# Kernel optimization log

Measured on AMD Instinct MI355X. Metric: run time of the kernel, lower is better.

The kernel has to match this reference:

```python
import jax, jax.numpy as jnp
import numpy as np

N, E, F, H, G = 50000, 1600000, 128, 128, 64
EPS = 1e-5  # BatchNorm eps


def setup_inputs() -> dict:
    key = jax.random.key(0)
    ks = jax.random.split(key, 16)
    x = jax.random.normal(ks[0], (N, F), dtype=jnp.float32)
    edge_index = jax.random.randint(ks[1], (2, E), 0, N, dtype=jnp.int64)
    batch = jnp.sort(jax.random.randint(ks[2], (N,), 0, G, dtype=jnp.int64))
    inp = {
        'x': x, 'edge_index': edge_index, 'batch': batch,
        'W1': jax.random.normal(ks[3], (F, H), dtype=jnp.float32) / np.sqrt(F),
        'b1': jnp.zeros((H,), jnp.float32),
        'bn1_gamma': jax.random.uniform(ks[4], (H,), jnp.float32, 0.5, 1.5),
        'bn1_beta': jax.random.normal(ks[5], (H,), jnp.float32) * 0.1,
        'bn1_mean': jax.random.normal(ks[6], (H,), jnp.float32) * 0.1,
        'bn1_var': jax.random.uniform(ks[7], (H,), jnp.float32, 0.5, 1.5),
        'W2': jax.random.normal(ks[8], (H, H), dtype=jnp.float32) / np.sqrt(H),
        'b2': jnp.zeros((H,), jnp.float32),
        'bn2_gamma': jax.random.uniform(ks[9], (H,), jnp.float32, 0.5, 1.5),
        'bn2_beta': jax.random.normal(ks[10], (H,), jnp.float32) * 0.1,
        'bn2_mean': jax.random.normal(ks[11], (H,), jnp.float32) * 0.1,
        'bn2_var': jax.random.uniform(ks[12], (H,), jnp.float32, 0.5, 1.5),
        'att_w': jax.random.normal(ks[13], (H, 1), dtype=jnp.float32) / np.sqrt(H),
        'cls_w': jax.random.normal(ks[14], (1, H), dtype=jnp.float32) / np.sqrt(H),
        'cls_b': jnp.zeros((1,), jnp.float32),
    }
    return inp


def gcn_conv(h, W, b, src, dst, n):
    # PyG GCNConv: linear, add self-loops, symmetric D^{-1/2}(A+I)D^{-1/2} aggregation, bias.
    hw = h @ W                                   # [n, H]
    loops = jnp.arange(n, dtype=src.dtype)
    s = jnp.concatenate([src, loops])
    d = jnp.concatenate([dst, loops])
    deg = jax.ops.segment_sum(jnp.ones_like(d, dtype=hw.dtype), d, num_segments=n)
    dis = jnp.where(deg > 0, jax.lax.rsqrt(deg), 0.0)
    norm = dis[s] * dis[d]                       # [E+n]
    msgs = hw[s] * norm[:, None]                 # gather + scale (memory-bound)
    return jax.ops.segment_sum(msgs, d, num_segments=n) + b


def batch_norm(h, gamma, beta, mean, var):
    return (h - mean) * gamma * jax.lax.rsqrt(var + EPS) + beta


def reference(x, edge_index, batch, W1, b1, bn1_gamma, bn1_beta, bn1_mean, bn1_var,
              W2, b2, bn2_gamma, bn2_beta, bn2_mean, bn2_var, att_w, cls_w, cls_b):
    n = x.shape[0]
    src, dst = edge_index[0], edge_index[1]
    # eval mode: dropout and edge-dropout are no-ops; BN uses running stats
    h = gcn_conv(x, W1, b1, src, dst, n)
    h = jax.nn.relu(batch_norm(h, bn1_gamma, bn1_beta, bn1_mean, bn1_var))
    h = gcn_conv(h, W2, b2, src, dst, n)
    h = jax.nn.relu(batch_norm(h, bn2_gamma, bn2_beta, bn2_mean, bn2_var))
    att = jax.nn.sigmoid(h @ att_w)              # [n, 1]
    g = jax.ops.segment_sum(h * att, batch, num_segments=G)  # [G, H]
    logits = g @ cls_w.T + cls_b                 # [G, 1]
    return logits, att
```

## Files before the change

kernel.cpp:

```cpp
#include <hip/hip_runtime.h>
#include <math.h>

#define NN 50000
#define HID 128
#define NG 64
#define BN_EPS 1e-5f

typedef __attribute__((ext_vector_type(8))) short short8;
typedef __attribute__((ext_vector_type(4))) float f32x4;

__device__ inline unsigned pack_bf2(float a, float b) {
    union { float f; unsigned u; } ua, ub;
    ua.f = a; ub.f = b;
    unsigned x = ua.u, y = ub.u;
    x += 0x7fffu + ((x >> 16) & 1u);
    y += 0x7fffu + ((y >> 16) & 1u);
    return (x >> 16) | (y & 0xffff0000u);
}
__device__ inline unsigned short bf16_1(float x) {
    union { float f; unsigned u; } v;
    v.f = x;
    unsigned r = v.u + 0x7fffu + ((v.u >> 16) & 1u);
    return (unsigned short)(r >> 16);
}
__device__ inline float2 unpack_bf2(unsigned v) {
    union { unsigned u; float f; } a, b;
    a.u = v << 16;
    b.u = v & 0xffff0000u;
    return make_float2(a.f, b.f);
}

#define NBKT 256
#define ETILE 8192
#define CAP   8192
#define ASTR 136

__global__ __launch_bounds__(128) void k_prep0(const float* __restrict__ W1,
                                               const float* __restrict__ W2,
                                               unsigned short* __restrict__ wt1,
                                               unsigned short* __restrict__ wt2,
                                               int* __restrict__ bcurP,
                                               const float* __restrict__ cls_b,
                                               float* __restrict__ logits) {
    int b = blockIdx.x;
    int t = threadIdx.x;
    if (b < 256) {
        int k = b & 127;
        const float* W = (b < 128) ? W1 : W2;
        unsigned short* wt = (b < 128) ? wt1 : wt2;
        wt[t * 128 + k] = bf16_1(W[k * 128 + t]);
    } else {
        #pragma unroll
        for (int i = 0; i < 32; ++i) bcurP[t * 32 + i] = 0;
        if (t < NG) logits[t] = cls_b[0];
    }
}

__global__ __launch_bounds__(256) void k_distribute(const int* __restrict__ src,
                                                    const int* __restrict__ dst,
                                                    int* __restrict__ bcurP,
                                                    unsigned* __restrict__ bpacked,
                                                    int E, int K) {
    __shared__ int h[NBKT];
    int t = threadIdx.x;
    h[t] = 0;
    __syncthreads();
    int base = blockIdx.x * ETILE;
    for (int i = 0; i < ETILE / 256; ++i) {
        int e = base + i * 256 + t;
        if (e < E) atomicAdd(&h[dst[e] / K], 1);
    }
    __syncthreads();
    int c = h[t];
    int my = (c > 0) ? atomicAdd(&bcurP[t * 16], c) : 0;
    __syncthreads();
    h[t] = my;
    __syncthreads();
    for (int i = 0; i < ETILE / 256; ++i) {
        int e = base + i * 256 + t;
        if (e < E) {
            int d = dst[e];
            int bkt = d / K;
            int p = atomicAdd(&h[bkt], 1);
            bpacked[(size_t)bkt * CAP + p] = ((unsigned)d << 16) | (unsigned)src[e];
        }
    }
}

__global__ __launch_bounds__(256) void k_csr_gemm1(const unsigned* __restrict__ bpacked,
                                                   const int* __restrict__ bcurP,
                                                   int* __restrict__ row_ptr,
                                                   int* __restrict__ degA,
                                                   float* __restrict__ dis,
                                                   int* __restrict__ col_idx,
                                                   const float* __restrict__ x,
                                                   const unsigned short* __restrict__ wt1,
                                                   unsigned short* __restrict__ zb,
                                                   int n, int K) {
    __shared__ unsigned short A[64][ASTR];
    __shared__ int cnt[NBKT];
    __shared__ int sA[NBKT];
    __shared__ int cur[NBKT];
    int t = threadIdx.x;
    int b = blockIdx.x;

    if (b >= NBKT) {
        int row0 = (b - NBKT) * 64;
        #pragma unroll
        for (int i = 0; i < 8; ++i) {
            int idx = t + i * 256;
            int r = idx >> 5;
            int c4 = (idx & 31) * 4;
            float4 v = make_float4(0.f, 0.f, 0.f, 0.f);
            if (row0 + r < n) v = *(const float4*)&x[(size_t)(row0 + r) * 128 + c4];
            uint2 p;
            p.x = pack_bf2(v.x, v.y);
            p.y = pack_bf2(v.z, v.w);
            *(uint2*)&A[r][c4] = p;
        }
        __syncthreads();
        int lane = t & 63;
        int wave = t >> 6;
        int m = lane & 15;
        int quad = lane >> 4;
        int r0 = wave * 16;
        short8 a[4];
        #pragma unroll
        for (int kt = 0; kt < 4; ++kt)
            a[kt] = *(const short8*)&A[r0 + m][kt * 32 + quad * 8];
        f32x4 acc[8];
        #pragma unroll
        for (int ct = 0; ct < 8; ++ct) acc[ct] = (f32x4){0.f, 0.f, 0.f, 0.f};
        short8 bcur[4], bnxt[4];
        {
            const unsigned short* wb = &wt1[(size_t)m * 128 + quad * 8];
            #pragma unroll
            for (int kt = 0; kt < 4; ++kt) bcur[kt] = *(const short8*)(wb + kt * 32);
        }
        #pragma unroll
        for (int ct = 0; ct < 8; ++ct) {
            if (ct < 7) {
                const unsigned short* wb = &wt1[(size_t)((ct + 1) * 16 + m) * 128 + quad * 8];
                #pragma unroll
                for (int kt = 0; kt < 4; ++kt) bnxt[kt] = *(const short8*)(wb + kt * 32);
            }
            #pragma unroll
            for (int kt = 0; kt < 4; ++kt)
                acc[ct] = __builtin_amdgcn_mfma_f32_16x16x32_bf16(a[kt], bcur[kt], acc[ct], 0, 0, 0);
            #pragma unroll
            for (int kt = 0; kt < 4; ++kt) bcur[kt] = bnxt[kt];
        }
        __syncthreads();
        #pragma unroll
        for (int ct = 0; ct < 8; ++ct) {
            int col = ct * 16 + m;
            #pragma unroll
            for (int reg = 0; reg < 4; ++reg)
                A[r0 + quad * 4 + reg][col] = bf16_1(acc[ct][reg]);
        }
        __syncthreads();
        #pragma unroll
        for (int i = 0; i < 4; ++i) {
            int idx = t + i * 256;
            int r = idx >> 4;
            int c8 = (idx & 15) * 8;
            int grow = row0 + r;
            if (grow < n)
                *(uint4*)&zb[(size_t)grow * 128 + c8] = *(const uint4*)&A[r][c8];
        }
        return;
    }

    int node0 = b * K;
    int nn = n - node0;
    if (nn > K) nn = K;
    if (nn < 0) nn = 0;
    int e0 = b * CAP;
    int e1 = e0 + bcurP[b * 16];
    cnt[t] = 0;
    __syncthreads();
    for (int e = e0 + t; e < e1; e += 256) {
        int ld = (int)(bpacked[e] >> 16) - node0;
        atomicAdd(&cnt[ld], 1);
    }
    __syncthreads();
    int c = cnt[t];
    sA[t] = c;
    __syncthreads();
    for (int off = 1; off < NBKT; off <<= 1) {
        int v = (t >= off) ? sA[t - off] : 0;
        __syncthreads();
        sA[t] += v;
        __syncthreads();
    }
    int rp = e0 + sA[t] - c;
    cur[t] = rp;
    if (t < nn) {
        row_ptr[node0 + t] = rp;
        degA[node0 + t] = c;
        dis[node0 + t] = rsqrtf((float)(c + 1));
    }
    __syncthreads();
    for (int e = e0 + t; e < e1; e += 256) {
        unsigned v = bpacked[e];
        int ld = (int)(v >> 16) - node0;
        int p = atomicAdd(&cur[ld], 1);
        col_idx[p] = (int)(v & 0xFFFFu);
    }
}


__device__ inline void gather4wide(const unsigned short* __restrict__ hwsb,
                                   const int* __restrict__ col_idx,
                                   int e0, int deg, int md,
                                   int sl, int part, bool active,
                                   float* acc8) {
    int cidx = (active && sl < deg) ? col_idx[e0 + sl] : 0;
    for (int it0 = 0; it0 < md; it0 += 16) {
        int nx = it0 + 16;
        int cidx_next = (active && (nx + sl) < deg && nx < md) ? col_idx[e0 + nx + sl] : 0;
        uint4 vv[16];
        #pragma unroll
        for (int j = 0; j < 16; ++j) {
            int s = __shfl(cidx, (part << 4) + j);
            vv[j] = (it0 + j < deg)
                        ? *(const uint4*)(hwsb + ((size_t)s << 7) + (sl << 3))
                        : make_uint4(0, 0, 0, 0);
        }
        #pragma unroll
        for (int j = 0; j < 16; ++j) {
            const unsigned* w = (const unsigned*)&vv[j];
            #pragma unroll
            for (int i2 = 0; i2 < 4; ++i2) {
                float2 f = unpack_bf2(w[i2]);
                acc8[2 * i2]     += f.x;
                acc8[2 * i2 + 1] += f.y;
            }
        }
        cidx = cidx_next;
    }
}

__device__ inline void gather4wide_scaled(const unsigned short* __restrict__ zb,
                                          const int* __restrict__ col_idx,
                                          const float* __restrict__ dis,
                                          int e0, int deg, int md,
                                          int sl, int part, bool active,
                                          float* acc8) {
    int cidx = (active && sl < deg) ? col_idx[e0 + sl] : 0;
    float cdis = (active && sl < deg) ? dis[cidx] : 0.f;
    for (int it0 = 0; it0 < md; it0 += 16) {
        int nx = it0 + 16;
        bool okn = (active && (nx + sl) < deg && nx < md);
        int cidx_next = okn ? col_idx[e0 + nx + sl] : 0;
        float cdis_next = okn ? dis[cidx_next] : 0.f;
        uint4 vv[16];
        float dsj[16];
        #pragma unroll
        for (int j = 0; j < 16; ++j) {
            int s = __shfl(cidx, (part << 4) + j);
            dsj[j] = __shfl(cdis, (part << 4) + j);
            vv[j] = (it0 + j < deg)
                        ? *(const uint4*)(zb + ((size_t)s << 7) + (sl << 3))
                        : make_uint4(0, 0, 0, 0);
        }
        #pragma unroll
        for (int j = 0; j < 16; ++j) {
            const unsigned* w = (const unsigned*)&vv[j];
            #pragma unroll
            for (int i2 = 0; i2 < 4; ++i2) {
                float2 f = unpack_bf2(w[i2]);
                acc8[2 * i2]     = fmaf(f.x, dsj[j], acc8[2 * i2]);
                acc8[2 * i2 + 1] = fmaf(f.y, dsj[j], acc8[2 * i2 + 1]);
            }
        }
        cidx = cidx_next;
        cdis = cdis_next;
    }
}


__global__ __launch_bounds__(256) void k_agg1_gemm2(const unsigned short* __restrict__ zb,
                                                    const int* __restrict__ row_ptr,
                                                    const int* __restrict__ degA,
                                                    const int* __restrict__ col_idx,
                                                    const float* __restrict__ dis,
                                                    const float* __restrict__ bias,
                                                    const float* __restrict__ gamma,
                                                    const float* __restrict__ beta,
                                                    const float* __restrict__ mean,
                                                    const float* __restrict__ var,
                                                    const unsigned short* __restrict__ wt2,
                                                    unsigned short* __restrict__ hwsb2, int n) {
    __shared__ unsigned short H1[16][ASTR];
    __shared__ unsigned short C2[16][ASTR];
    int t = threadIdx.x;
    int wave = t >> 6, lane = t & 63;
    int sl = lane & 15, part = lane >> 4;
    int d = blockIdx.x * 16 + wave * 4 + part;
    bool active = (d < n);
    int e0 = 0, deg = 0;
    if (active) {
        e0 = row_ptr[d];
        deg = degA[d];
    }
    int md = deg;
    md = max(md, __shfl_xor(md, 16));
    md = max(md, __shfl_xor(md, 32));

    float acc8[8] = {0, 0, 0, 0, 0, 0, 0, 0};
    gather4wide_scaled(zb, col_idx, dis, e0, deg, md, sl, part, active, acc8);

    unsigned outw[4] = {0, 0, 0, 0};
    if (active) {
        float dd = dis[d];
        uint4 v = *(const uint4*)(zb + ((size_t)d << 7) + (sl << 3));
        const unsigned* w = (const unsigned*)&v;
        #pragma unroll
        for (int i2 = 0; i2 < 4; ++i2) {
            float2 f = unpack_bf2(w[i2]);
            acc8[2 * i2]     = fmaf(f.x, dd, acc8[2 * i2]);
            acc8[2 * i2 + 1] = fmaf(f.y, dd, acc8[2 * i2 + 1]);
        }
        int f0 = sl << 3;
        #pragma unroll
        for (int i2 = 0; i2 < 4; ++i2) {
            int f = f0 + 2 * i2;
            float2 bv = *(const float2*)&bias[f];
            float2 gm = *(const float2*)&gamma[f];
            float2 bt = *(const float2*)&beta[f];
            float2 mn = *(const float2*)&mean[f];
            float2 vr = *(const float2*)&var[f];
            float vx = acc8[2 * i2] * dd + bv.x;
            float vy = acc8[2 * i2 + 1] * dd + bv.y;
            float sx = gm.x * rsqrtf(vr.x + BN_EPS);
            float sy = gm.y * rsqrtf(vr.y + BN_EPS);
            float rx = fmaxf((vx - mn.x) * sx + bt.x, 0.f);
            float ry = fmaxf((vy - mn.y) * sy + bt.y, 0.f);
            outw[i2] = pack_bf2(rx, ry);
        }
    }
    int local = wave * 4 + part;
    *(uint4*)&H1[local][sl << 3] = *(uint4*)outw;
    __syncthreads();

    int m = sl;
    int quad = part;
    short8 a2[4];
    #pragma unroll
    for (int kt = 0; kt < 4; ++kt)
        a2[kt] = *(const short8*)&H1[m][kt * 32 + quad * 8];

    f32x4 acc2[2];
    acc2[0] = (f32x4){0.f, 0.f, 0.f, 0.f};
    acc2[1] = (f32x4){0.f, 0.f, 0.f, 0.f};
    #pragma unroll
    for (int i = 0; i < 2; ++i) {
        int ct = wave * 2 + i;
        const unsigned short* wb = &wt2[(size_t)(ct * 16 + m) * 128 + quad * 8];
        #pragma unroll
        for (int kt = 0; kt < 4; ++kt) {
            short8 b = *(const short8*)(wb + kt * 32);
            acc2[i] = __builtin_amdgcn_mfma_f32_16x16x32_bf16(a2[kt], b, acc2[i], 0, 0, 0);
        }
    }
    int gr = blockIdx.x * 16 + quad * 4;
    float ds2[4];
    #pragma unroll
    for (int reg = 0; reg < 4; ++reg)
        ds2[reg] = (gr + reg < n) ? dis[gr + reg] : 0.f;
    #pragma unroll
    for (int i = 0; i < 2; ++i) {
        int col = (wave * 2 + i) * 16 + m;
        #pragma unroll
        for (int reg = 0; reg < 4; ++reg)
            C2[quad * 4 + reg][col] = bf16_1(acc2[i][reg] * ds2[reg]);
    }
    __syncthreads();
    {
        int r = t >> 4;
        int c8 = (t & 15) * 8;
        int grow = blockIdx.x * 16 + r;
        if (grow < n)
            *(uint4*)&hwsb2[(size_t)grow * 128 + c8] = *(const uint4*)&C2[r][c8];
    }
}


__global__ __launch_bounds__(256) void k_agg2_att_logit(const unsigned short* __restrict__ hwsb,
                                                        const int* __restrict__ row_ptr,
                                                        const int* __restrict__ degA,
                                                        const int* __restrict__ col_idx,
                                                        const float* __restrict__ dis,
                                                        const float* __restrict__ bias,
                                                        const float* __restrict__ gamma,
                                                        const float* __restrict__ beta,
                                                        const float* __restrict__ mean,
                                                        const float* __restrict__ var,
                                                        const int* __restrict__ batch,
                                                        const float* __restrict__ att_w,
                                                        const float* __restrict__ cls_w,
                                                        float* __restrict__ att_out,
                                                        float* __restrict__ logits, int n) {
    __shared__ int   sg[16];
    __shared__ float sv[16];
    int t = threadIdx.x;
    int wave = t >> 6, lane = t & 63;
    int sl = lane & 15, part = lane >> 4;
    int d = blockIdx.x * 16 + wave * 4 + part;
    bool active = (d < n);
    int e0 = 0, deg = 0;
    if (active) {
        e0 = row_ptr[d];
        deg = degA[d];
    }
    int md = deg;
    md = max(md, __shfl_xor(md, 16));
    md = max(md, __shfl_xor(md, 32));

    float acc8[8] = {0, 0, 0, 0, 0, 0, 0, 0};
    gather4wide(hwsb, col_idx, e0, deg, md, sl, part, active, acc8);

    int g = -1;
    float contrib = 0.f;
    float p = 0.f, q = 0.f;
    if (active) {
        uint4 v = *(const uint4*)(hwsb + ((size_t)d << 7) + (sl << 3));
        const unsigned* w = (const unsigned*)&v;
        #pragma unroll
        for (int i2 = 0; i2 < 4; ++i2) {
            float2 f = unpack_bf2(w[i2]);
            acc8[2 * i2]     += f.x;
            acc8[2 * i2 + 1] += f.y;
        }
        float dd = dis[d];
        int f0 = sl << 3;
        #pragma unroll
        for (int i2 = 0; i2 < 4; ++i2) {
            int f = f0 + 2 * i2;
            float2 bv = *(const float2*)&bias[f];
            float2 gm = *(const float2*)&gamma[f];
            float2 bt = *(const float2*)&beta[f];
            float2 mn = *(const float2*)&mean[f];
            float2 vr = *(const float2*)&var[f];
            float vx = acc8[2 * i2] * dd + bv.x;
            float vy = acc8[2 * i2 + 1] * dd + bv.y;
            float sx = gm.x * rsqrtf(vr.x + BN_EPS);
            float sy = gm.y * rsqrtf(vr.y + BN_EPS);
            float rx = fmaxf((vx - mn.x) * sx + bt.x, 0.f);
            float ry = fmaxf((vy - mn.y) * sy + bt.y, 0.f);
            float2 aw = *(const float2*)&att_w[f];
            float2 cw = *(const float2*)&cls_w[f];
            p += rx * aw.x + ry * aw.y;
            q += rx * cw.x + ry * cw.y;
        }
    }
    #pragma unroll
    for (int off = 1; off < 16; off <<= 1) {
        p += __shfl_xor(p, off);
        q += __shfl_xor(q, off);
    }
    if (active) {
        float a = 1.f / (1.f + expf(-p));
        if (sl == 0) att_out[d] = a;
        g = batch[d];
        contrib = a * q;
    }
    if (sl == 0) {
        sg[wave * 4 + part] = g;
        sv[wave * 4 + part] = contrib;
    }
    __syncthreads();
    if (t == 0) {
        int cur = -1;
        float acc = 0.f;
        #pragma unroll
        for (int i = 0; i < 16; ++i) {
            int gi = sg[i];
            if (gi < 0) continue;
            if (gi != cur) {
                if (cur >= 0) atomicAdd(&logits[cur], acc);
                cur = gi;
                acc = 0.f;
            }
            acc += sv[i];
        }
        if (cur >= 0) atomicAdd(&logits[cur], acc);
    }
}


extern "C" void kernel_launch(void* const* d_in, const int* in_sizes, int n_in,
                              void* d_out, int out_size, void* d_ws, size_t ws_size,
                              hipStream_t stream) {
    const float* x   = (const float*)d_in[0];
    const int*   ei  = (const int*)d_in[1];
    const int*   bat = (const int*)d_in[2];
    const float* W1  = (const float*)d_in[3];
    const float* b1  = (const float*)d_in[4];
    const float* g1  = (const float*)d_in[5];
    const float* bt1 = (const float*)d_in[6];
    const float* mn1 = (const float*)d_in[7];
    const float* vr1 = (const float*)d_in[8];
    const float* W2  = (const float*)d_in[9];
    const float* b2  = (const float*)d_in[10];
    const float* g2  = (const float*)d_in[11];
    const float* bt2 = (const float*)d_in[12];
    const float* mn2 = (const float*)d_in[13];
    const float* vr2 = (const float*)d_in[14];
    const float* attw = (const float*)d_in[15];
    const float* clsw = (const float*)d_in[16];
    const float* clsb = (const float*)d_in[17];

    int E = in_sizes[1] / 2;
    int n = in_sizes[2];
    const int* src = ei;
    const int* dst = ei + E;
    int K = (n + NBKT - 1) / NBKT;

    char* ws = (char*)d_ws;
    auto alloc = [&](size_t bytes) {
        void* p = (void*)ws;
        ws += (bytes + 255) & ~(size_t)255;
        return p;
    };
    int*            bcurP   = (int*)alloc(NBKT * 16 * 4);
    unsigned*       bpacked = (unsigned*)alloc((size_t)NBKT * CAP * 4);
    int*            row_ptr = (int*)alloc((size_t)n * 4);
    int*            degA    = (int*)alloc((size_t)n * 4);
    int*            col_idx = (int*)alloc((size_t)NBKT * CAP * 4);
    float*          dis     = (float*)alloc((size_t)n * 4);
    unsigned short* zb      = (unsigned short*)alloc((size_t)n * 128 * 2);
    unsigned short* hwsb2   = (unsigned short*)alloc((size_t)n * 128 * 2);
    unsigned short* wt1     = (unsigned short*)alloc(128 * 128 * 2);
    unsigned short* wt2     = (unsigned short*)alloc(128 * 128 * 2);

    float* out = (float*)d_out;
    int etiles = (E + ETILE - 1) / ETILE;
    int gb = (n + 63) / 64;
    int ab = (n + 15) / 16;

    k_prep0<<<257, 128, 0, stream>>>(W1, W2, wt1, wt2, bcurP, clsb, out);
    k_distribute<<<etiles, 256, 0, stream>>>(src, dst, bcurP, bpacked, E, K);
    k_csr_gemm1<<<NBKT + gb, 256, 0, stream>>>(bpacked, bcurP, row_ptr, degA, dis,
                                               col_idx, x, wt1, zb, n, K);
    k_agg1_gemm2<<<ab, 256, 0, stream>>>(zb, row_ptr, degA, col_idx, dis,
                                         b1, g1, bt1, mn1, vr1, wt2, hwsb2, n);
    k_agg2_att_logit<<<ab, 256, 0, stream>>>(hwsb2, row_ptr, degA, col_idx, dis,
                                             b2, g2, bt2, mn2, vr2, bat, attw, clsw,
                                             out + NG, out, n);
}
```

Baseline: 287.6 us.

## Stage bucketed edges in shared memory and flush coalesced chunks in distribute

Replaces the two-pass count-then-scatter edge distribution with a single pass. Each block stages packed edges per bucket in LDS buffers, with a direct global atomic fallback on overflow. Full 16-entry groups are flushed with vectorized contiguous writes. The aim is to avoid the second read of dst and the scattered 4-byte global stores. The cost is more block-wide syncs, more global atomics, and edge order within a bucket that can vary between runs.

```diff
diff --git a/kernel.cpp b/kernel.cpp
--- a/kernel.cpp
+++ b/kernel.cpp
@@ -31,9 +31,11 @@
 }
 
 #define NBKT 256
-#define ETILE 8192
 #define CAP   8192
 #define ASTR 136
+#define DBUF  48
+#define DBATCH 2048
+#define DBLOCKS 192
 
 __global__ __launch_bounds__(128) void k_prep0(const float* __restrict__ W1,
                                                const float* __restrict__ W2,
@@ -58,32 +60,65 @@
 
 __global__ __launch_bounds__(256) void k_distribute(const int* __restrict__ src,
                                                     const int* __restrict__ dst,
-                                                    int* __restrict__ bcurP,
+                                                    int* __restrict__ gcurP,
                                                     unsigned* __restrict__ bpacked,
                                                     int E, int K) {
-    __shared__ int h[NBKT];
+    __shared__ unsigned buf[NBKT][DBUF];
+    __shared__ int cnt[NBKT];
     int t = threadIdx.x;
-    h[t] = 0;
-    __syncthreads();
-    int base = blockIdx.x * ETILE;
-    for (int i = 0; i < ETILE / 256; ++i) {
-        int e = base + i * 256 + t;
-        if (e < E) atomicAdd(&h[dst[e] / K], 1);
-    }
-    __syncthreads();
-    int c = h[t];
-    int my = (c > 0) ? atomicAdd(&bcurP[t * 16], c) : 0;
-    __syncthreads();
-    h[t] = my;
-    __syncthreads();
-    for (int i = 0; i < ETILE / 256; ++i) {
-        int e = base + i * 256 + t;
-        if (e < E) {
+    cnt[t] = 0;
+    __syncthreads();
+    int per = (E + gridDim.x - 1) / gridDim.x;
+    int s0 = blockIdx.x * per;
+    int s1 = s0 + per;
+    if (s1 > E) s1 = E;
+    for (int base = s0; base < s1; base += DBATCH) {
+        int lim = base + DBATCH;
+        if (lim > s1) lim = s1;
+        for (int e = base + t; e < lim; e += 256) {
             int d = dst[e];
             int bkt = d / K;
-            int p = atomicAdd(&h[bkt], 1);
-            bpacked[(size_t)bkt * CAP + p] = ((unsigned)d << 16) | (unsigned)src[e];
-        }
+            unsigned pk = ((unsigned)d << 16) | (unsigned)src[e];
+            int pos = atomicAdd(&cnt[bkt], 1);
+            if (pos < DBUF) {
+                buf[bkt][pos] = pk;
+            } else {
+                int p = atomicAdd(&gcurP[bkt * 16], 1);
+                bpacked[(size_t)bkt * CAP + p] = pk;
+            }
+        }
+        __syncthreads();
+        int c = cnt[t];
+        if (c > DBUF) c = DBUF;
+        int f = c & ~15;
+        if (f > 0) {
+            int b0 = atomicAdd(&gcurP[t * 16], f);
+            unsigned* gp = bpacked + (size_t)t * CAP + b0;
+            if ((b0 & 3) == 0) {
+                for (int i = 0; i < f; i += 4) {
+                    uint4 v = make_uint4(buf[t][i], buf[t][i + 1], buf[t][i + 2], buf[t][i + 3]);
+                    *(uint4*)(gp + i) = v;
+                }
+            } else {
+                for (int i = 0; i < f; ++i) gp[i] = buf[t][i];
+            }
+            for (int i = 0; i < c - f; ++i) buf[t][i] = buf[t][f + i];
+        }
+        cnt[t] = c - f;
+        __syncthreads();
+    }
+    int c = cnt[t];
+    if (c > DBUF) c = DBUF;
+    if (c > 0) {
+        int b0 = atomicAdd(&gcurP[t * 16], c);
+        unsigned* gp = bpacked + (size_t)t * CAP + b0;
+        int i = 0;
+        if ((b0 & 3) == 0)
+            for (; i + 4 <= c; i += 4) {
+                uint4 v = make_uint4(buf[t][i], buf[t][i + 1], buf[t][i + 2], buf[t][i + 3]);
+                *(uint4*)(gp + i) = v;
+            }
+        for (; i < c; ++i) gp[i] = buf[t][i];
     }
 }
 
@@ -536,12 +571,11 @@
     unsigned short* wt2     = (unsigned short*)alloc(128 * 128 * 2);
 
     float* out = (float*)d_out;
-    int etiles = (E + ETILE - 1) / ETILE;
     int gb = (n + 63) / 64;
     int ab = (n + 15) / 16;
 
     k_prep0<<<257, 128, 0, stream>>>(W1, W2, wt1, wt2, bcurP, clsb, out);
-    k_distribute<<<etiles, 256, 0, stream>>>(src, dst, bcurP, bpacked, E, K);
+    k_distribute<<<DBLOCKS, 256, 0, stream>>>(src, dst, bcurP, bpacked, E, K);
     k_csr_gemm1<<<NBKT + gb, 256, 0, stream>>>(bpacked, bcurP, row_ptr, degA, dis,
                                                col_idx, x, wt1, zb, n, K);
     k_agg1_gemm2<<<ab, 256, 0, stream>>>(zb, row_ptr, degA, col_idx, dis,
```

Result: faster. 281.4 us (-2.2%).
